# Kernel optimization log

Hardware: AMD Instinct MI355X
Metric: run time of the kernel (lower is better)

## Reference

```python
import jax, jax.numpy as jnp
import numpy as np

N_NODES = 131072
IN_F = 512
HID = 512
H = 8
DH = HID // H
B = 1024  # batch_size (num graphs); static for jit
LN_EPS = 1e-5


def setup_inputs() -> dict:
    key = jax.random.key(0)
    ks = jax.random.split(key, 12)
    # equal-size segments (128 nodes/graph), sorted as in PyG batching
    batch = (jnp.arange(N_NODES) // (N_NODES // B)).astype(jnp.int32)
    s = 0.02
    return {
        "x": jax.random.normal(ks[0], (N_NODES, IN_F), jnp.float32),
        "batch": batch,
        "query": jax.random.normal(ks[1], (H, DH), jnp.float32) * s,
        "key_w": jax.random.normal(ks[2], (HID, IN_F), jnp.float32) * s,
        "key_b": jnp.zeros((HID,), jnp.float32),
        "value_w": jax.random.normal(ks[3], (HID, IN_F), jnp.float32) * s,
        "value_b": jnp.zeros((HID,), jnp.float32),
        "out_w": jax.random.normal(ks[4], (IN_F, HID), jnp.float32) * s,
        "out_b": jnp.zeros((IN_F,), jnp.float32),
        "gate_w": jax.random.normal(ks[5], (IN_F, 2 * IN_F), jnp.float32) * s,
        "gate_b": jnp.zeros((IN_F,), jnp.float32),
        "ln_w": jnp.ones((IN_F,), jnp.float32),
        "ln_b": jnp.zeros((IN_F,), jnp.float32),
    }


def reference(x, batch, query, key_w, key_b, value_w, value_b, out_w, out_b,
              gate_w, gate_b, ln_w, ln_b):
    N = x.shape[0]
    # projections (dense GEMMs)
    keys = (x @ key_w.T + key_b).reshape(N, H, DH)
    values = (x @ value_w.T + value_b).reshape(N, H, DH)
    # per-node attention logits against shared per-head query: [N, H]
    scores = jnp.einsum('nhd,hd->nh', keys, query)
    # segment softmax over nodes within each graph
    smax = jax.ops.segment_max(scores, batch, num_segments=B)  # [B, H]
    smax = jnp.where(jnp.isfinite(smax), smax, 0.0)            # guard empty graphs
    e = jnp.exp(scores - smax[batch])
    ssum = jax.ops.segment_sum(e, batch, num_segments=B)       # [B, H]
    w = e / jnp.maximum(ssum[batch], 1e-12)                    # [N, H]  (dropout is eval-mode identity)
    # attention-weighted pooling of values: [B, H, DH] -> [B, HID]
    pooled = jax.ops.segment_sum(w[:, :, None] * values, batch, num_segments=B)
    ctx = pooled.reshape(B, HID) @ out_w.T + out_b             # [B, IN_F]
    # gating with per-graph mean pool
    counts = jax.ops.segment_sum(jnp.ones((N,), x.dtype), batch, num_segments=B)
    avg = jax.ops.segment_sum(x, batch, num_segments=B) / jnp.maximum(counts, 1.0)[:, None]
    gate = jax.nn.sigmoid(jnp.concatenate([ctx, avg], axis=1) @ gate_w.T + gate_b)
    ctx = gate * ctx + (1.0 - gate) * avg
    emb = jnp.where(counts[:, None] > 0, ctx, 0.0)             # empty graphs stay zero
    # LayerNorm
    mu = emb.mean(-1, keepdims=True)
    var = emb.var(-1, keepdims=True)
    return (emb - mu) / jnp.sqrt(var + LN_EPS) * ln_w + ln_b
```

## Files before the change

kernel.cpp:

```cpp
#include <hip/hip_runtime.h>
#include <hip/hip_bf16.h>

typedef short short8 __attribute__((ext_vector_type(8)));
typedef float f32x4 __attribute__((ext_vector_type(4)));

#define NGRAPH 1024
#define NPG    128
#define INF    512
#define NHEAD  8
#define CH     32

__device__ __forceinline__ ushort f2b(float f){
  __hip_bfloat16 h(f);
  union { __hip_bfloat16 h; ushort u; } v; v.h = h; return v.u;
}
__device__ __forceinline__ float b2f_lo(unsigned u){
  union { unsigned u; float f; } v; v.u = u << 16; return v.f;
}
__device__ __forceinline__ float b2f_hi(unsigned u){
  union { unsigned u; float f; } v; v.u = u & 0xffff0000u; return v.f;
}

__global__ void k_kq(const float* __restrict__ q, const float* __restrict__ kw,
                     float* __restrict__ kq){
  int h = blockIdx.x, t = threadIdx.x;
  float s = 0.f;
  #pragma unroll 8
  for(int d = 0; d < 64; d++)
    s += q[h*64 + d] * kw[(size_t)(h*64 + d)*INF + t];
  kq[h*INF + t] = s;
}

__global__ __launch_bounds__(128, 2) void k_graph(
    const float* __restrict__ x, const float* __restrict__ kq,
    const float* __restrict__ vw, const float* __restrict__ ow,
    const float* __restrict__ gw,
    ushort* __restrict__ vwb, ushort* __restrict__ owb, ushort* __restrict__ gwb,
    ushort* __restrict__ xw_b, float* __restrict__ avg_f, ushort* __restrict__ avg_b){
  __shared__ __align__(16) ushort xs[CH*INF];
  __shared__ __align__(16) float  sc[CH*NHEAD];
  __shared__ float mEf[3*NHEAD];

  const int t = threadIdx.x, lane = t & 63, w = t >> 6;
  const int col = lane & 15, kg = lane >> 4;
  const int g = blockIdx.x;
  const int node = w*16 + col;

  {
    int idx = g*1024 + t*8;
    const float* src; ushort* dst; int off;
    if(idx < 262144){ src = vw; dst = vwb; off = idx; }
    else if(idx < 524288){ src = ow; dst = owb; off = idx - 262144; }
    else { src = gw; dst = gwb; off = idx - 524288; }
    float4 a = *(const float4*)(src + off);
    float4 b = *(const float4*)(src + off + 4);
    short8 v;
    v[0]=(short)f2b(a.x); v[1]=(short)f2b(a.y); v[2]=(short)f2b(a.z); v[3]=(short)f2b(a.w);
    v[4]=(short)f2b(b.x); v[5]=(short)f2b(b.y); v[6]=(short)f2b(b.z); v[7]=(short)f2b(b.w);
    *(short8*)(dst + off) = v;
  }

  short8 bfrag[16];
  {
    const bool ok = (col < 8);
    const float* kqr = kq + col*INF;
    #pragma unroll
    for(int ks = 0; ks < 16; ks++){
      short8 v = short8{0,0,0,0,0,0,0,0};
      if(ok){
        float4 p0 = *(const float4*)(kqr + ks*32 + kg*8);
        float4 p1 = *(const float4*)(kqr + ks*32 + kg*8 + 4);
        v[0]=(short)f2b(p0.x); v[1]=(short)f2b(p0.y); v[2]=(short)f2b(p0.z); v[3]=(short)f2b(p0.w);
        v[4]=(short)f2b(p1.x); v[5]=(short)f2b(p1.y); v[6]=(short)f2b(p1.z); v[7]=(short)f2b(p1.w);
      }
      bfrag[ks] = v;
    }
  }

  if(t < NHEAD){ mEf[t] = -1e30f; mEf[NHEAD + t] = 0.f; }

  float4 pf[16];
  {
    const float* xr = x + (size_t)(g*NPG + node)*INF + kg*8;
    #pragma unroll
    for(int ks = 0; ks < 8; ks++){
      pf[2*ks]     = *(const float4*)(xr + ks*32);
      pf[2*ks + 1] = *(const float4*)(xr + ks*32 + 4);
    }
  }

  float2 acc2[NHEAD][2];
  #pragma unroll
  for(int h = 0; h < NHEAD; h++){
    acc2[h][0] = float2{0.f, 0.f}; acc2[h][1] = float2{0.f, 0.f};
  }
  float2 cs01 = {0.f, 0.f}, cs23 = {0.f, 0.f};

  for(int c = 0; c < 4; c++){
    {
      const float* xr = x + (size_t)(g*NPG + c*CH + node)*INF + kg*8;
      f32x4 sacc = {0.f,0.f,0.f,0.f};
      #pragma unroll
      for(int ks = 0; ks < 16; ks++){
        float4 a, b;
        if(ks < 8){ a = pf[2*ks]; b = pf[2*ks + 1]; }
        else { a = *(const float4*)(xr + ks*32); b = *(const float4*)(xr + ks*32 + 4); }
        short8 af;
        af[0]=(short)f2b(a.x); af[1]=(short)f2b(a.y); af[2]=(short)f2b(a.z); af[3]=(short)f2b(a.w);
        af[4]=(short)f2b(b.x); af[5]=(short)f2b(b.y); af[6]=(short)f2b(b.z); af[7]=(short)f2b(b.w);
        *(short8*)((char*)xs + node*1024 + ((ks*64 + kg*16) ^ ((node & 7) << 4))) = af;
        sacc = __builtin_amdgcn_mfma_f32_16x16x32_bf16(af, bfrag[ks], sacc, 0, 0, 0);
      }
      if(col < 8){
        #pragma unroll
        for(int r = 0; r < 4; r++)
          sc[(w*16 + kg*4 + r)*NHEAD + col] = sacc[r];
      }
    }
    __syncthreads();

    {
      int h = t >> 4, s = t & 15;
      float v[2]; float m = -1e30f;
      #pragma unroll
      for(int i = 0; i < 2; i++){ v[i] = sc[(s + 16*i)*NHEAD + h]; m = fmaxf(m, v[i]); }
      #pragma unroll
      for(int msk = 1; msk < 16; msk <<= 1) m = fmaxf(m, __shfl_xor(m, msk));
      float es = 0.f;
      #pragma unroll
      for(int i = 0; i < 2; i++){ v[i] = __expf(v[i] - m); es += v[i]; }
      #pragma unroll
      for(int msk = 1; msk < 16; msk <<= 1) es += __shfl_xor(es, msk);
      float M = mEf[h], E = mEf[NHEAD + h];
      float Mn = fmaxf(M, m);
      float f_old = __expf(M - Mn), f_new = __expf(m - Mn);
      #pragma unroll
      for(int i = 0; i < 2; i++) sc[(s + 16*i)*NHEAD + h] = v[i]*f_new;
      if(s == 0){
        mEf[h] = Mn;
        mEf[NHEAD + h] = E*f_old + es*f_new;
        mEf[2*NHEAD + h] = f_old;
      }
    }
    __syncthreads();

    {
      float fo[NHEAD];
      #pragma unroll
      for(int h = 0; h < NHEAD; h++) fo[h] = mEf[2*NHEAD + h];
      #pragma unroll
      for(int h = 0; h < NHEAD; h++){
        acc2[h][0].x *= fo[h]; acc2[h][0].y *= fo[h];
        acc2[h][1].x *= fo[h]; acc2[h][1].y *= fo[h];
      }
      if(c < 3){
        const float* xn = x + (size_t)(g*NPG + (c+1)*CH + node)*INF + kg*8;
        #pragma unroll
        for(int ks = 0; ks < 8; ks++){
          pf[2*ks]     = *(const float4*)(xn + ks*32);
          pf[2*ks + 1] = *(const float4*)(xn + ks*32 + 4);
        }
      }
      #pragma unroll 4
      for(int n = 0; n < CH; n++){
        uint2 xv = *(const uint2*)((const char*)xs + n*1024 + ((8*t) ^ ((n & 7) << 4)));
        float2 x01 = {b2f_lo(xv.x), b2f_hi(xv.x)};
        float2 x23 = {b2f_lo(xv.y), b2f_hi(xv.y)};
        float4 w0 = *(float4*)(sc + n*NHEAD);
        float4 w1 = *(float4*)(sc + n*NHEAD + 4);
        float wv[8] = {w0.x, w0.y, w0.z, w0.w, w1.x, w1.y, w1.z, w1.w};
        #pragma unroll
        for(int h = 0; h < NHEAD; h++){
          acc2[h][0].x = fmaf(wv[h], x01.x, acc2[h][0].x);
          acc2[h][0].y = fmaf(wv[h], x01.y, acc2[h][0].y);
          acc2[h][1].x = fmaf(wv[h], x23.x, acc2[h][1].x);
          acc2[h][1].y = fmaf(wv[h], x23.y, acc2[h][1].y);
        }
        cs01.x += x01.x; cs01.y += x01.y; cs23.x += x23.x; cs23.y += x23.y;
      }
    }
    __syncthreads();
  }

  #pragma unroll
  for(int h = 0; h < NHEAD; h++){
    float einv = 1.0f / fmaxf(mEf[NHEAD + h], 1e-12f);
    float v0 = acc2[h][0].x*einv, v1 = acc2[h][0].y*einv;
    float v2 = acc2[h][1].x*einv, v3 = acc2[h][1].y*einv;
    uint2 pk = { (unsigned)f2b(v0) | ((unsigned)f2b(v1) << 16),
                 (unsigned)f2b(v2) | ((unsigned)f2b(v3) << 16) };
    *(uint2*)(xw_b + (size_t)g*4096 + h*INF + 4*t) = pk;
  }
  float am0 = cs01.x*(1.0f/128.0f), am1 = cs01.y*(1.0f/128.0f);
  float am2 = cs23.x*(1.0f/128.0f), am3 = cs23.y*(1.0f/128.0f);
  float4 av = {am0, am1, am2, am3};
  *(float4*)(avg_f + (size_t)g*INF + 4*t) = av;
  uint2 pk = { (unsigned)f2b(am0) | ((unsigned)f2b(am1) << 16),
               (unsigned)f2b(am2) | ((unsigned)f2b(am3) << 16) };
  *(uint2*)(avg_b + (size_t)g*INF + 4*t) = pk;
}

__global__ __launch_bounds__(256, 4) void gemm_tn(
    const ushort* __restrict__ A1, const ushort* __restrict__ A2,
    int lda, int headmode,
    const ushort* __restrict__ Wt, int ldw,
    const float* __restrict__ bias,
    float* __restrict__ Cf, ushort* __restrict__ Cb,
    int ldc, int K, int ksplit){
  __shared__ ushort As[2][64*72];
  __shared__ ushort Bs[2][32*72];
  const int t = threadIdx.x, lane = t & 63, w = t >> 6;
  const int m0 = blockIdx.x*64, n0 = blockIdx.y*32;
  const int aoff = headmode ? (blockIdx.y >> 1)*512 : 0;
  const int col = lane & 15, kg = lane >> 4;
  const int ar = t >> 2, ak = (t & 3)*16;
  const int br = t >> 3, bk = (t & 7)*8;

  f32x4 acc[2];
  acc[0] = f32x4{0.f,0.f,0.f,0.f};
  acc[1] = f32x4{0.f,0.f,0.f,0.f};

  const ushort* Ap0 = (0 < ksplit) ? A1 : A2;
  short8 va0 = *(const short8*)(Ap0 + (size_t)(m0 + ar)*lda + aoff + ak);
  short8 va1 = *(const short8*)(Ap0 + (size_t)(m0 + ar)*lda + aoff + ak + 8);
  short8 vb  = *(const short8*)(Wt + (size_t)(n0 + br)*ldw + bk);
  int buf = 0;
  for(int kc = 0; kc < K; kc += 64){
    *(short8*)((char*)&As[buf][0] + ar*144 + ak*2)      = va0;
    *(short8*)((char*)&As[buf][0] + ar*144 + ak*2 + 16) = va1;
    *(short8*)((char*)&Bs[buf][0] + br*144 + bk*2)      = vb;
    __syncthreads();
    if(kc + 64 < K){
      int kn = kc + 64;
      const ushort* Ap = (kn < ksplit) ? A1 : A2;
      int kl = (kn < ksplit) ? kn : kn - ksplit;
      va0 = *(const short8*)(Ap + (size_t)(m0 + ar)*lda + aoff + kl + ak);
      va1 = *(const short8*)(Ap + (size_t)(m0 + ar)*lda + aoff + kl + ak + 8);
      vb  = *(const short8*)(Wt + (size_t)(n0 + br)*ldw + kn + bk);
    }
    const int mr = (w & 1)*32, nc = (w >> 1)*16;
    #pragma unroll
    for(int kk = 0; kk < 2; kk++){
      short8 af0 = *(short8*)((char*)&As[buf][0] + (mr + col)*144      + kk*64 + kg*16);
      short8 af1 = *(short8*)((char*)&As[buf][0] + (mr + 16 + col)*144 + kk*64 + kg*16);
      short8 bf  = *(short8*)((char*)&Bs[buf][0] + (nc + col)*144      + kk*64 + kg*16);
      acc[0] = __builtin_amdgcn_mfma_f32_16x16x32_bf16(af0, bf, acc[0], 0,0,0);
      acc[1] = __builtin_amdgcn_mfma_f32_16x16x32_bf16(af1, bf, acc[1], 0,0,0);
    }
    buf ^= 1;
  }
  #pragma unroll
  for(int mi = 0; mi < 2; mi++)
    #pragma unroll
    for(int r = 0; r < 4; r++){
      int rr = m0 + (w & 1)*32 + mi*16 + kg*4 + r;
      int cc = n0 + (w >> 1)*16 + col;
      float vv = acc[mi][r] + bias[cc];
      if(Cf) Cf[(size_t)rr*ldc + cc] = vv;
      if(Cb) Cb[(size_t)rr*ldc + cc] = f2b(vv);
    }
}

__global__ __launch_bounds__(512, 2) void k5_epilogue(
    const float* __restrict__ z, const float* __restrict__ ctx,
    const float* __restrict__ avg, const float* __restrict__ lnw,
    const float* __restrict__ lnb, float* __restrict__ out){
  __shared__ float red[16];
  const int t = threadIdx.x, b = blockIdx.x;
  const size_t i = (size_t)b*INF + t;
  float zz = z[i], c = ctx[i], a = avg[i];
  float g = 1.0f / (1.0f + __expf(-zz));
  float e = g*c + (1.0f - g)*a;
  float s1 = e, s2 = e*e;
  #pragma unroll
  for(int m = 1; m < 64; m <<= 1){ s1 += __shfl_xor(s1, m); s2 += __shfl_xor(s2, m); }
  int wv = t >> 6;
  if((t & 63) == 0){ red[wv] = s1; red[8 + wv] = s2; }
  __syncthreads();
  float ts1 = 0.f, ts2 = 0.f;
  #pragma unroll
  for(int k = 0; k < 8; k++){ ts1 += red[k]; ts2 += red[8 + k]; }
  float mu = ts1 * (1.0f/512.0f);
  float var = ts2 * (1.0f/512.0f) - mu*mu;
  out[i] = (e - mu) * rsqrtf(var + 1e-5f) * lnw[t] + lnb[t];
}

extern "C" void kernel_launch(void* const* d_in, const int* in_sizes, int n_in,
                              void* d_out, int out_size, void* d_ws, size_t ws_size,
                              hipStream_t stream){
  const float* x       = (const float*)d_in[0];
  const float* query   = (const float*)d_in[2];
  const float* key_w   = (const float*)d_in[3];
  const float* value_w = (const float*)d_in[5];
  const float* value_b = (const float*)d_in[6];
  const float* out_w   = (const float*)d_in[7];
  const float* out_b   = (const float*)d_in[8];
  const float* gate_w  = (const float*)d_in[9];
  const float* gate_b  = (const float*)d_in[10];
  const float* ln_w    = (const float*)d_in[11];
  const float* ln_b    = (const float*)d_in[12];
  float* out = (float*)d_out;

  char* ws = (char*)d_ws;
  float*  kq       = (float*) (ws + 0);
  ushort* vw_b     = (ushort*)(ws + 16384);
  ushort* ow_b     = (ushort*)(ws + 540672);
  ushort* gw_b     = (ushort*)(ws + 1064960);
  ushort* xw_b     = (ushort*)(ws + 2113536);
  float*  avg_f    = (float*) (ws + 10502144);
  ushort* avg_b    = (ushort*)(ws + 12599296);
  ushort* pooled_b = (ushort*)(ws + 13647872);
  float*  ctx_f    = (float*) (ws + 14696448);
  ushort* ctx_b    = (ushort*)(ws + 16793600);
  float*  z_f      = (float*) (ws + 17842176);

  k_kq<<<8, 512, 0, stream>>>(query, key_w, kq);

  k_graph<<<NGRAPH, 128, 0, stream>>>(x, kq, value_w, out_w, gate_w,
                                      vw_b, ow_b, gw_b, xw_b, avg_f, avg_b);

  gemm_tn<<<dim3(16, 16), 256, 0, stream>>>(xw_b, xw_b, 4096, 1, vw_b, 512, value_b,
                                            nullptr, pooled_b, 512, 512, 1 << 30);
  gemm_tn<<<dim3(16, 16), 256, 0, stream>>>(pooled_b, pooled_b, 512, 0, ow_b, 512, out_b,
                                            ctx_f, ctx_b, 512, 512, 1 << 30);
  gemm_tn<<<dim3(16, 16), 256, 0, stream>>>(ctx_b, avg_b, 512, 0, gw_b, 1024, gate_b,
                                            z_f, nullptr, 512, 1024, 512);

  k5_epilogue<<<NGRAPH, 512, 0, stream>>>(z_f, ctx_f, avg_f, ln_w, ln_b, out);
}
```

Before: 94.37 us.

## Halve chunk size, split K across waves, drop register prefetch for occupancy

The chunk of nodes processed per iteration shrinks from 32 to 16, and the two waves now split the 512-wide feature dimension of each node's score dot-product instead of splitting nodes. Partial scores go to a new shared buffer and are summed before the online softmax. The register prefetch of the next chunk's x rows is removed and launch bounds rise to 4 blocks per SM, trading explicit load/compute overlap for lower register and LDS pressure and higher occupancy. The price is twice as many chunk iterations and barriers per graph.

```diff
diff --git a/kernel.cpp b/kernel.cpp
--- a/kernel.cpp
+++ b/kernel.cpp
@@ -8,7 +8,7 @@
 #define NPG    128
 #define INF    512
 #define NHEAD  8
-#define CH     32
+#define CH     16
 
 __device__ __forceinline__ ushort f2b(float f){
   __hip_bfloat16 h(f);
@@ -31,20 +31,20 @@
   kq[h*INF + t] = s;
 }
 
-__global__ __launch_bounds__(128, 2) void k_graph(
+__global__ __launch_bounds__(128, 4) void k_graph(
     const float* __restrict__ x, const float* __restrict__ kq,
     const float* __restrict__ vw, const float* __restrict__ ow,
     const float* __restrict__ gw,
     ushort* __restrict__ vwb, ushort* __restrict__ owb, ushort* __restrict__ gwb,
     ushort* __restrict__ xw_b, float* __restrict__ avg_f, ushort* __restrict__ avg_b){
   __shared__ __align__(16) ushort xs[CH*INF];
+  __shared__ __align__(16) float  scp[2*CH*NHEAD];
   __shared__ __align__(16) float  sc[CH*NHEAD];
   __shared__ float mEf[3*NHEAD];
 
   const int t = threadIdx.x, lane = t & 63, w = t >> 6;
   const int col = lane & 15, kg = lane >> 4;
   const int g = blockIdx.x;
-  const int node = w*16 + col;
 
   {
     int idx = g*1024 + t*8;
@@ -60,12 +60,12 @@
     *(short8*)(dst + off) = v;
   }
 
-  short8 bfrag[16];
+  short8 bfrag[8];
   {
     const bool ok = (col < 8);
-    const float* kqr = kq + col*INF;
+    const float* kqr = kq + col*INF + w*256;
     #pragma unroll
-    for(int ks = 0; ks < 16; ks++){
+    for(int ks = 0; ks < 8; ks++){
       short8 v = short8{0,0,0,0,0,0,0,0};
       if(ok){
         float4 p0 = *(const float4*)(kqr + ks*32 + kg*8);
@@ -79,16 +79,6 @@
 
   if(t < NHEAD){ mEf[t] = -1e30f; mEf[NHEAD + t] = 0.f; }
 
-  float4 pf[16];
-  {
-    const float* xr = x + (size_t)(g*NPG + node)*INF + kg*8;
-    #pragma unroll
-    for(int ks = 0; ks < 8; ks++){
-      pf[2*ks]     = *(const float4*)(xr + ks*32);
-      pf[2*ks + 1] = *(const float4*)(xr + ks*32 + 4);
-    }
-  }
-
   float2 acc2[NHEAD][2];
   #pragma unroll
   for(int h = 0; h < NHEAD; h++){
@@ -96,46 +86,41 @@
   }
   float2 cs01 = {0.f, 0.f}, cs23 = {0.f, 0.f};
 
-  for(int c = 0; c < 4; c++){
+  for(int c = 0; c < 8; c++){
     {
-      const float* xr = x + (size_t)(g*NPG + c*CH + node)*INF + kg*8;
+      const float* xr = x + (size_t)(g*NPG + c*CH + col)*INF + w*256 + kg*8;
       f32x4 sacc = {0.f,0.f,0.f,0.f};
       #pragma unroll
-      for(int ks = 0; ks < 16; ks++){
-        float4 a, b;
-        if(ks < 8){ a = pf[2*ks]; b = pf[2*ks + 1]; }
-        else { a = *(const float4*)(xr + ks*32); b = *(const float4*)(xr + ks*32 + 4); }
+      for(int ks = 0; ks < 8; ks++){
+        float4 a = *(const float4*)(xr + ks*32);
+        float4 b = *(const float4*)(xr + ks*32 + 4);
         short8 af;
         af[0]=(short)f2b(a.x); af[1]=(short)f2b(a.y); af[2]=(short)f2b(a.z); af[3]=(short)f2b(a.w);
         af[4]=(short)f2b(b.x); af[5]=(short)f2b(b.y); af[6]=(short)f2b(b.z); af[7]=(short)f2b(b.w);
-        *(short8*)((char*)xs + node*1024 + ((ks*64 + kg*16) ^ ((node & 7) << 4))) = af;
+        *(short8*)((char*)xs + col*1024 + (((w*8 + ks)*64 + kg*16) ^ ((col & 7) << 4))) = af;
         sacc = __builtin_amdgcn_mfma_f32_16x16x32_bf16(af, bfrag[ks], sacc, 0, 0, 0);
       }
       if(col < 8){
         #pragma unroll
         for(int r = 0; r < 4; r++)
-          sc[(w*16 + kg*4 + r)*NHEAD + col] = sacc[r];
+          scp[w*128 + (kg*4 + r)*NHEAD + col] = sacc[r];
       }
     }
     __syncthreads();
 
     {
       int h = t >> 4, s = t & 15;
-      float v[2]; float m = -1e30f;
-      #pragma unroll
-      for(int i = 0; i < 2; i++){ v[i] = sc[(s + 16*i)*NHEAD + h]; m = fmaxf(m, v[i]); }
+      float v = scp[s*NHEAD + h] + scp[128 + s*NHEAD + h];
+      float m = v;
       #pragma unroll
       for(int msk = 1; msk < 16; msk <<= 1) m = fmaxf(m, __shfl_xor(m, msk));
-      float es = 0.f;
-      #pragma unroll
-      for(int i = 0; i < 2; i++){ v[i] = __expf(v[i] - m); es += v[i]; }
+      float e = __expf(v - m), es = e;
       #pragma unroll
       for(int msk = 1; msk < 16; msk <<= 1) es += __shfl_xor(es, msk);
       float M = mEf[h], E = mEf[NHEAD + h];
       float Mn = fmaxf(M, m);
       float f_old = __expf(M - Mn), f_new = __expf(m - Mn);
-      #pragma unroll
-      for(int i = 0; i < 2; i++) sc[(s + 16*i)*NHEAD + h] = v[i]*f_new;
+      sc[s*NHEAD + h] = e*f_new;
       if(s == 0){
         mEf[h] = Mn;
         mEf[NHEAD + h] = E*f_old + es*f_new;
@@ -152,14 +137,6 @@
       for(int h = 0; h < NHEAD; h++){
         acc2[h][0].x *= fo[h]; acc2[h][0].y *= fo[h];
         acc2[h][1].x *= fo[h]; acc2[h][1].y *= fo[h];
-      }
-      if(c < 3){
-        const float* xn = x + (size_t)(g*NPG + (c+1)*CH + node)*INF + kg*8;
-        #pragma unroll
-        for(int ks = 0; ks < 8; ks++){
-          pf[2*ks]     = *(const float4*)(xn + ks*32);
-          pf[2*ks + 1] = *(const float4*)(xn + ks*32 + 4);
-        }
       }
       #pragma unroll 4
       for(int n = 0; n < CH; n++){
```

Result: slower. 107.9 us (+14.4%).

## Replace LDS-staged GEMM with direct global-to-register MFMA loads

Applied to the files above, without the earlier changes.

The small 1024x512 GEMMs drop LDS double-buffering and barriers. Each wave now loads its MFMA A and B fragments straight from global memory (mostly L2) and computes a 16x32 tile. This removes LDS traffic and __syncthreads, at the cost of redundant global loads of weight rows across waves and less coalesced per-lane access.

```diff
diff --git a/kernel.cpp b/kernel.cpp
--- a/kernel.cpp
+++ b/kernel.cpp
@@ -200,65 +200,42 @@
   *(uint2*)(avg_b + (size_t)g*INF + 4*t) = pk;
 }
 
-__global__ __launch_bounds__(256, 4) void gemm_tn(
+__global__ __launch_bounds__(256) void gemm_direct(
     const ushort* __restrict__ A1, const ushort* __restrict__ A2,
     int lda, int headmode,
     const ushort* __restrict__ Wt, int ldw,
     const float* __restrict__ bias,
     float* __restrict__ Cf, ushort* __restrict__ Cb,
     int ldc, int K, int ksplit){
-  __shared__ ushort As[2][64*72];
-  __shared__ ushort Bs[2][32*72];
   const int t = threadIdx.x, lane = t & 63, w = t >> 6;
-  const int m0 = blockIdx.x*64, n0 = blockIdx.y*32;
+  const int col = lane & 15, kg = lane >> 4;
+  const int m0 = blockIdx.x*64 + w*16, n0 = blockIdx.y*32;
   const int aoff = headmode ? (blockIdx.y >> 1)*512 : 0;
-  const int col = lane & 15, kg = lane >> 4;
-  const int ar = t >> 2, ak = (t & 3)*16;
-  const int br = t >> 3, bk = (t & 7)*8;
-
-  f32x4 acc[2];
-  acc[0] = f32x4{0.f,0.f,0.f,0.f};
-  acc[1] = f32x4{0.f,0.f,0.f,0.f};
-
-  const ushort* Ap0 = (0 < ksplit) ? A1 : A2;
-  short8 va0 = *(const short8*)(Ap0 + (size_t)(m0 + ar)*lda + aoff + ak);
-  short8 va1 = *(const short8*)(Ap0 + (size_t)(m0 + ar)*lda + aoff + ak + 8);
-  short8 vb  = *(const short8*)(Wt + (size_t)(n0 + br)*ldw + bk);
-  int buf = 0;
-  for(int kc = 0; kc < K; kc += 64){
-    *(short8*)((char*)&As[buf][0] + ar*144 + ak*2)      = va0;
-    *(short8*)((char*)&As[buf][0] + ar*144 + ak*2 + 16) = va1;
-    *(short8*)((char*)&Bs[buf][0] + br*144 + bk*2)      = vb;
-    __syncthreads();
-    if(kc + 64 < K){
-      int kn = kc + 64;
-      const ushort* Ap = (kn < ksplit) ? A1 : A2;
-      int kl = (kn < ksplit) ? kn : kn - ksplit;
-      va0 = *(const short8*)(Ap + (size_t)(m0 + ar)*lda + aoff + kl + ak);
-      va1 = *(const short8*)(Ap + (size_t)(m0 + ar)*lda + aoff + kl + ak + 8);
-      vb  = *(const short8*)(Wt + (size_t)(n0 + br)*ldw + kn + bk);
-    }
-    const int mr = (w & 1)*32, nc = (w >> 1)*16;
-    #pragma unroll
-    for(int kk = 0; kk < 2; kk++){
-      short8 af0 = *(short8*)((char*)&As[buf][0] + (mr + col)*144      + kk*64 + kg*16);
-      short8 af1 = *(short8*)((char*)&As[buf][0] + (mr + 16 + col)*144 + kk*64 + kg*16);
-      short8 bf  = *(short8*)((char*)&Bs[buf][0] + (nc + col)*144      + kk*64 + kg*16);
-      acc[0] = __builtin_amdgcn_mfma_f32_16x16x32_bf16(af0, bf, acc[0], 0,0,0);
-      acc[1] = __builtin_amdgcn_mfma_f32_16x16x32_bf16(af1, bf, acc[1], 0,0,0);
-    }
-    buf ^= 1;
-  }
-  #pragma unroll
-  for(int mi = 0; mi < 2; mi++)
-    #pragma unroll
-    for(int r = 0; r < 4; r++){
-      int rr = m0 + (w & 1)*32 + mi*16 + kg*4 + r;
-      int cc = n0 + (w >> 1)*16 + col;
-      float vv = acc[mi][r] + bias[cc];
-      if(Cf) Cf[(size_t)rr*ldc + cc] = vv;
-      if(Cb) Cb[(size_t)rr*ldc + cc] = f2b(vv);
-    }
+
+  f32x4 acc0 = {0.f,0.f,0.f,0.f}, acc1 = {0.f,0.f,0.f,0.f};
+  const ushort* wr0 = Wt + (size_t)(n0 + col)*ldw + kg*8;
+  const ushort* wr1 = Wt + (size_t)(n0 + 16 + col)*ldw + kg*8;
+
+  #pragma unroll 8
+  for(int ks = 0; ks < K/32; ks++){
+    int kk = ks*32 + kg*8;
+    const ushort* Ap = (kk < ksplit) ? A1 : A2;
+    int kl = (kk < ksplit) ? kk : kk - ksplit;
+    short8 af  = *(const short8*)(Ap + (size_t)(m0 + col)*lda + aoff + kl);
+    short8 bf0 = *(const short8*)(wr0 + ks*32);
+    short8 bf1 = *(const short8*)(wr1 + ks*32);
+    acc0 = __builtin_amdgcn_mfma_f32_16x16x32_bf16(af, bf0, acc0, 0,0,0);
+    acc1 = __builtin_amdgcn_mfma_f32_16x16x32_bf16(af, bf1, acc1, 0,0,0);
+  }
+  #pragma unroll
+  for(int r = 0; r < 4; r++){
+    int rr = m0 + kg*4 + r;
+    int c0 = n0 + col, c1 = n0 + 16 + col;
+    float v0 = acc0[r] + bias[c0];
+    float v1 = acc1[r] + bias[c1];
+    if(Cf){ Cf[(size_t)rr*ldc + c0] = v0; Cf[(size_t)rr*ldc + c1] = v1; }
+    if(Cb){ Cb[(size_t)rr*ldc + c0] = f2b(v0); Cb[(size_t)rr*ldc + c1] = f2b(v1); }
+  }
 }
 
 __global__ __launch_bounds__(512, 2) void k5_epilogue(
@@ -319,12 +296,12 @@
   k_graph<<<NGRAPH, 128, 0, stream>>>(x, kq, value_w, out_w, gate_w,
                                       vw_b, ow_b, gw_b, xw_b, avg_f, avg_b);
 
-  gemm_tn<<<dim3(16, 16), 256, 0, stream>>>(xw_b, xw_b, 4096, 1, vw_b, 512, value_b,
-                                            nullptr, pooled_b, 512, 512, 1 << 30);
-  gemm_tn<<<dim3(16, 16), 256, 0, stream>>>(pooled_b, pooled_b, 512, 0, ow_b, 512, out_b,
-                                            ctx_f, ctx_b, 512, 512, 1 << 30);
-  gemm_tn<<<dim3(16, 16), 256, 0, stream>>>(ctx_b, avg_b, 512, 0, gw_b, 1024, gate_b,
-                                            z_f, nullptr, 512, 1024, 512);
+  gemm_direct<<<dim3(16, 16), 256, 0, stream>>>(xw_b, xw_b, 4096, 1, vw_b, 512, value_b,
+                                                nullptr, pooled_b, 512, 512, 1 << 30);
+  gemm_direct<<<dim3(16, 16), 256, 0, stream>>>(pooled_b, pooled_b, 512, 0, ow_b, 512, out_b,
+                                                ctx_f, ctx_b, 512, 512, 1 << 30);
+  gemm_direct<<<dim3(16, 16), 256, 0, stream>>>(ctx_b, avg_b, 512, 0, gw_b, 1024, gate_b,
+                                                z_f, nullptr, 512, 1024, 512);
 
   k5_epilogue<<<NGRAPH, 512, 0, stream>>>(z_f, ctx_f, avg_f, ln_w, ln_b, out);
 }
```

Result: slower. 101.2 us (+7.3%).

## Fuse gate GEMM with sigmoid gating and LayerNorm epilogue

Applied to the files above, without the earlier changes.

Replaces the separate gate GEMM launch and the per-row epilogue kernel with one kernel. Each block takes 16 graph rows, stages the concatenated ctx/avg bf16 rows in swizzled LDS, runs MFMA against gate weights read straight from global memory, keeps z in shared memory, then applies the sigmoid gate and LayerNorm. This removes one launch and the z round trip through global memory. In exchange only 64 blocks are launched and the gate weights are streamed from global/L2 without LDS tiling, so the GEMM may be latency-bound.

```diff
diff --git a/kernel.cpp b/kernel.cpp
--- a/kernel.cpp
+++ b/kernel.cpp
@@ -261,28 +261,79 @@
     }
 }
 
-__global__ __launch_bounds__(512, 2) void k5_epilogue(
-    const float* __restrict__ z, const float* __restrict__ ctx,
-    const float* __restrict__ avg, const float* __restrict__ lnw,
-    const float* __restrict__ lnb, float* __restrict__ out){
-  __shared__ float red[16];
-  const int t = threadIdx.x, b = blockIdx.x;
-  const size_t i = (size_t)b*INF + t;
-  float zz = z[i], c = ctx[i], a = avg[i];
-  float g = 1.0f / (1.0f + __expf(-zz));
-  float e = g*c + (1.0f - g)*a;
-  float s1 = e, s2 = e*e;
+__global__ __launch_bounds__(256, 2) void k_zln(
+    const ushort* __restrict__ ctxb, const ushort* __restrict__ avgb,
+    const ushort* __restrict__ gwb, const float* __restrict__ gb,
+    const float* __restrict__ ctxf, const float* __restrict__ avgf,
+    const float* __restrict__ lnw, const float* __restrict__ lnb,
+    float* __restrict__ out){
+  __shared__ __align__(16) ushort As[16*1024];
+  __shared__ __align__(16) float  zf[16*512];
+  const int t = threadIdx.x, lane = t & 63, w = t >> 6;
+  const int col = lane & 15, kg = lane >> 4;
+  const int r0 = blockIdx.x*16;
+
   #pragma unroll
-  for(int m = 1; m < 64; m <<= 1){ s1 += __shfl_xor(s1, m); s2 += __shfl_xor(s2, m); }
-  int wv = t >> 6;
-  if((t & 63) == 0){ red[wv] = s1; red[8 + wv] = s2; }
+  for(int it = 0; it < 8; it++){
+    int i = it*2048 + t*8;
+    int row = i >> 10, k = i & 1023;
+    short8 v;
+    if(k < 512) v = *(const short8*)(ctxb + (size_t)(r0 + row)*512 + k);
+    else        v = *(const short8*)(avgb + (size_t)(r0 + row)*512 + (k - 512));
+    *(short8*)((char*)As + row*2048 + ((k*2) ^ ((row & 7) << 4))) = v;
+  }
   __syncthreads();
-  float ts1 = 0.f, ts2 = 0.f;
-  #pragma unroll
-  for(int k = 0; k < 8; k++){ ts1 += red[k]; ts2 += red[8 + k]; }
-  float mu = ts1 * (1.0f/512.0f);
-  float var = ts2 * (1.0f/512.0f) - mu*mu;
-  out[i] = (e - mu) * rsqrtf(var + 1e-5f) * lnw[t] + lnb[t];
+
+  {
+    f32x4 zacc[8];
+    #pragma unroll
+    for(int ni = 0; ni < 8; ni++) zacc[ni] = f32x4{0.f,0.f,0.f,0.f};
+    for(int ks = 0; ks < 32; ks++){
+      int kk = ks*32 + kg*8;
+      short8 af = *(short8*)((char*)As + col*2048 + ((kk*2) ^ ((col & 7) << 4)));
+      #pragma unroll
+      for(int ni = 0; ni < 8; ni++){
+        short8 bf = *(const short8*)(gwb + (size_t)((w*8 + ni)*16 + col)*1024 + kk);
+        zacc[ni] = __builtin_amdgcn_mfma_f32_16x16x32_bf16(af, bf, zacc[ni], 0,0,0);
+      }
+    }
+    #pragma unroll
+    for(int ni = 0; ni < 8; ni++)
+      #pragma unroll
+      for(int r = 0; r < 4; r++){
+        int row = kg*4 + r, cc = (w*8 + ni)*16 + col;
+        zf[row*512 + cc] = zacc[ni][r] + gb[cc];
+      }
+  }
+  __syncthreads();
+
+  {
+    const int row = t >> 4, j = t & 15;
+    float e[32];
+    float s1 = 0.f, s2 = 0.f;
+    #pragma unroll
+    for(int i = 0; i < 32; i++){
+      int cc = j + i*16;
+      float zz = zf[row*512 + cc];
+      float cv = ctxf[(size_t)(r0 + row)*512 + cc];
+      float av = avgf[(size_t)(r0 + row)*512 + cc];
+      float gg = 1.0f / (1.0f + __expf(-zz));
+      float ee = gg*cv + (1.0f - gg)*av;
+      e[i] = ee; s1 += ee; s2 += ee*ee;
+    }
+    #pragma unroll
+    for(int msk = 1; msk < 16; msk <<= 1){
+      s1 += __shfl_xor(s1, msk); s2 += __shfl_xor(s2, msk);
+    }
+    float mu = s1*(1.0f/512.0f);
+    float var = s2*(1.0f/512.0f) - mu*mu;
+    float rinv = rsqrtf(var + 1e-5f);
+    #pragma unroll
+    for(int i = 0; i < 32; i++){
+      int cc = j + i*16;
+      out[(size_t)(r0 + row)*512 + cc] = (e[i] - mu)*rinv*lnw[cc] + lnb[cc];
+    }
+  }
 }
 
 extern "C" void kernel_launch(void* const* d_in, const int* in_sizes, int n_in,
@@ -312,7 +363,6 @@
   ushort* pooled_b = (ushort*)(ws + 13647872);
   float*  ctx_f    = (float*) (ws + 14696448);
   ushort* ctx_b    = (ushort*)(ws + 16793600);
-  float*  z_f      = (float*) (ws + 17842176);
 
   k_kq<<<8, 512, 0, stream>>>(query, key_w, kq);
 
@@ -323,8 +373,6 @@
                                             nullptr, pooled_b, 512, 512, 1 << 30);
   gemm_tn<<<dim3(16, 16), 256, 0, stream>>>(pooled_b, pooled_b, 512, 0, ow_b, 512, out_b,
                                             ctx_f, ctx_b, 512, 512, 1 << 30);
-  gemm_tn<<<dim3(16, 16), 256, 0, stream>>>(ctx_b, avg_b, 512, 0, gw_b, 1024, gate_b,
-                                            z_f, nullptr, 512, 1024, 512);
-
-  k5_epilogue<<<NGRAPH, 512, 0, stream>>>(z_f, ctx_f, avg_f, ln_w, ln_b, out);
-}
+  k_zln<<<64, 256, 0, stream>>>(ctx_b, avg_b, gw_b, gate_b, ctx_f, avg_f,
+                                ln_w, ln_b, out);
+}
```

New measurement: 114.0 us. 1.21x slower.
